# Performance work log

Measured on AMD Instinct MI355X. Metric: run time of the kernel, lower is better.

The kernel has to match this reference:

```python
import jax, jax.numpy as jnp
import numpy as np

D_MODEL = 1024
NUM_HEADS = 16
HEAD_DIM = D_MODEL // NUM_HEADS
FF_DIM = 4096
MAX_SEQ_LEN = 5000
EPS = 1e-5


def setup_inputs() -> dict:
    key = jax.random.key(0)
    ks = jax.random.split(key, 16)
    B, S = 2, 2048
    s = 0.02
    inp = {
        'x': jax.random.normal(ks[0], (B, S, D_MODEL), dtype=jnp.float32),
        'mask': jnp.ones((B, 1, S, S), dtype=jnp.int32),
        # attention projections (stored as (in, out); y = x @ W + b)
        'wq': jax.random.normal(ks[1], (D_MODEL, D_MODEL), jnp.float32) * s,
        'bq': jnp.zeros((D_MODEL,), jnp.float32),
        'wk': jax.random.normal(ks[2], (D_MODEL, D_MODEL), jnp.float32) * s,
        'bk': jnp.zeros((D_MODEL,), jnp.float32),
        'wv': jax.random.normal(ks[3], (D_MODEL, D_MODEL), jnp.float32) * s,
        'bv': jnp.zeros((D_MODEL,), jnp.float32),
        'wo': jax.random.normal(ks[4], (D_MODEL, D_MODEL), jnp.float32) * s,
        'bo': jnp.zeros((D_MODEL,), jnp.float32),
        # FFN
        'w1': jax.random.normal(ks[5], (D_MODEL, FF_DIM), jnp.float32) * s,
        'b1': jnp.zeros((FF_DIM,), jnp.float32),
        'w2': jax.random.normal(ks[6], (FF_DIM, D_MODEL), jnp.float32) * s,
        'b2': jnp.zeros((D_MODEL,), jnp.float32),
        # layer norms
        'g1': jnp.ones((D_MODEL,), jnp.float32),
        'be1': jnp.zeros((D_MODEL,), jnp.float32),
        'g2': jnp.ones((D_MODEL,), jnp.float32),
        'be2': jnp.zeros((D_MODEL,), jnp.float32),
        # relative position bias table: (2*max_seq_len-1, num_heads)
        'bias_table': jax.random.normal(ks[7], (2 * MAX_SEQ_LEN - 1, NUM_HEADS), jnp.float32) * s,
    }
    return inp


def _layer_norm(x, g, b):
    mu = jnp.mean(x, axis=-1, keepdims=True)
    var = jnp.mean(jnp.square(x - mu), axis=-1, keepdims=True)
    return (x - mu) / jnp.sqrt(var + EPS) * g + b


def reference(x, mask, wq, bq, wk, bk, wv, bv, wo, bo,
              w1, b1, w2, b2, g1, be1, g2, be2, bias_table):
    B, S, _ = x.shape
    # --- pre-norm attention block ---
    residual = x
    xn = _layer_norm(x, g1, be1)

    # relative position bias, computed on-the-fly: (S, S, H)
    coords = jnp.arange(S)
    rel = coords[:, None] - coords[None, :] + (MAX_SEQ_LEN - 1)
    rel = jnp.clip(rel, 0, 2 * MAX_SEQ_LEN - 2)
    rel_bias = bias_table[rel]  # (S, S, H)

    q = (xn @ wq + bq).reshape(B, S, NUM_HEADS, HEAD_DIM)
    k = (xn @ wk + bk).reshape(B, S, NUM_HEADS, HEAD_DIM)
    v = (xn @ wv + bv).reshape(B, S, NUM_HEADS, HEAD_DIM)

    scores = jnp.einsum('bqhd,bkhd->bhqk', q, k) / jnp.sqrt(jnp.float32(HEAD_DIM))
    # torch: scores + bias.unsqueeze(0).transpose(1,3) -> adds bias[k, q, h]
    scores = scores + jnp.transpose(rel_bias, (2, 1, 0))[None]
    scores = jnp.where(mask == 0, jnp.float32(-1e9), scores)
    attn = jax.nn.softmax(scores, axis=-1)
    ctx = jnp.einsum('bhqk,bkhd->bqhd', attn, v).reshape(B, S, D_MODEL)
    attn_out = ctx @ wo + bo
    x = residual + attn_out

    # --- pre-norm FFN block ---
    residual = x
    xn = _layer_norm(x, g2, be2)
    h = jax.nn.gelu(xn @ w1 + b1, approximate=False)
    x = residual + (h @ w2 + b2)
    return x
```

## Files before the change

kernel.cpp:

```cpp
#include <hip/hip_runtime.h>
#include <hip/hip_bf16.h>
#include <math.h>

#define S_LEN 2048
#define DM 1024
#define NH 16
#define HD 64
#define FF 4096
#define MAXSEQ 5000
#define QS 3072

typedef __attribute__((ext_vector_type(8))) short bf16x8;
typedef __attribute__((ext_vector_type(4))) float f32x4;

__device__ __forceinline__ void async_copy16(const void* g, void* l) {
    __builtin_amdgcn_global_load_lds(
        (const __attribute__((address_space(1))) void*)g,
        (__attribute__((address_space(3))) void*)l, 16, 0, 0);
}

__device__ __forceinline__ short f2bf_s(float v) {
    __hip_bfloat16 h = __float2bfloat16(v);
    return *reinterpret_cast<short*>(&h);
}

__device__ __forceinline__ float gelu_fast(float v) {
    float u = 0.7978845608f * (v + 0.044715f * v * v * v);
    float e = __expf(2.0f * u);
    float th = 1.0f - 2.0f / (e + 1.0f);
    return 0.5f * v * (1.0f + th);
}

__global__ __launch_bounds__(256) void ln_bf16_kernel(
    const float* __restrict__ x, const float* __restrict__ g,
    const float* __restrict__ be, __hip_bfloat16* __restrict__ out)
{
    int row = blockIdx.x;
    int t = threadIdx.x;
    const float* xr = x + (size_t)row * DM;
    float v[4];
    float s = 0.f, sq = 0.f;
#pragma unroll
    for (int i = 0; i < 4; i++) {
        v[i] = xr[t + 256 * i];
        s += v[i];
        sq += v[i] * v[i];
    }
    __shared__ float rs[256], rs2[256];
    rs[t] = s; rs2[t] = sq;
    __syncthreads();
    for (int off = 128; off > 0; off >>= 1) {
        if (t < off) { rs[t] += rs[t + off]; rs2[t] += rs2[t + off]; }
        __syncthreads();
    }
    float mu = rs[0] * (1.0f / DM);
    float var = rs2[0] * (1.0f / DM) - mu * mu;
    float rstd = rsqrtf(var + 1e-5f);
    __hip_bfloat16* orow = out + (size_t)row * DM;
#pragma unroll
    for (int i = 0; i < 4; i++) {
        int c = t + 256 * i;
        orow[c] = __float2bfloat16((v[i] - mu) * rstd * g[c] + be[c]);
    }
}

__global__ __launch_bounds__(256) void reduce_ln_kernel(
    const float* __restrict__ P0, const float* __restrict__ P1,
    const float* __restrict__ bo, const float* __restrict__ x,
    const float* __restrict__ g, const float* __restrict__ be,
    float* __restrict__ out, __hip_bfloat16* __restrict__ xn)
{
    int row = blockIdx.x;
    int t = threadIdx.x;
    size_t base = (size_t)row * DM;
    float v[4];
    float s = 0.f, sq = 0.f;
#pragma unroll
    for (int i = 0; i < 4; i++) {
        int c = t + 256 * i;
        float val = P0[base + c] + P1[base + c] + bo[c] + x[base + c];
        out[base + c] = val;
        v[i] = val;
        s += val;
        sq += val * val;
    }
    __shared__ float rs[256], rs2[256];
    rs[t] = s; rs2[t] = sq;
    __syncthreads();
    for (int off = 128; off > 0; off >>= 1) {
        if (t < off) { rs[t] += rs[t + off]; rs2[t] += rs2[t + off]; }
        __syncthreads();
    }
    float mu = rs[0] * (1.0f / DM);
    float var = rs2[0] * (1.0f / DM) - mu * mu;
    float rstd = rsqrtf(var + 1e-5f);
#pragma unroll
    for (int i = 0; i < 4; i++) {
        int c = t + 256 * i;
        xn[base + c] = __float2bfloat16((v[i] - mu) * rstd * g[c] + be[c]);
    }
}

__global__ __launch_bounds__(256) void reduce2_kernel(
    const float4* __restrict__ P0, const float4* __restrict__ P1,
    const float* __restrict__ b2, float* __restrict__ out)
{
    int f = blockIdx.x * 256 + threadIdx.x;
    float4 a = P0[f], b = P1[f];
    float4 r = ((const float4*)out)[f];
    float4 bb = ((const float4*)b2)[f & 255];
    float4 o;
    o.x = r.x + a.x + b.x + bb.x;
    o.y = r.y + a.y + b.y + bb.y;
    o.z = r.z + a.z + b.z + bb.z;
    o.w = r.w + a.w + b.w + bb.w;
    ((float4*)out)[f] = o;
}

__global__ __launch_bounds__(256) void prep_kernel(
    const float* __restrict__ wq, const float* __restrict__ wk,
    const float* __restrict__ wv, const float* __restrict__ wo,
    const float* __restrict__ w1, const float* __restrict__ w2,
    const float* __restrict__ bq, const float* __restrict__ bk,
    const float* __restrict__ bv,
    __hip_bfloat16* __restrict__ WqkvT, __hip_bfloat16* __restrict__ WoT,
    __hip_bfloat16* __restrict__ W1T, __hip_bfloat16* __restrict__ W2T,
    float* __restrict__ bqkv)
{
    int blk = blockIdx.x;
    if (blk >= 12288) {
        int i = (blk - 12288) * 256 + threadIdx.x;
        float v = (i < 1024) ? bq[i] : (i < 2048 ? bk[i - 1024] : bv[i - 2048]);
        bqkv[i] = v;
        return;
    }
    const float* W; __hip_bfloat16* Wt; int K, N, tbase;
    if (blk < 1024)      { W = wq; Wt = WqkvT;                      K = 1024; N = 1024; tbase = 0; }
    else if (blk < 2048) { W = wk; Wt = WqkvT + (size_t)1024 * DM;  K = 1024; N = 1024; tbase = 1024; }
    else if (blk < 3072) { W = wv; Wt = WqkvT + (size_t)2048 * DM;  K = 1024; N = 1024; tbase = 2048; }
    else if (blk < 4096) { W = wo; Wt = WoT;                        K = 1024; N = 1024; tbase = 3072; }
    else if (blk < 8192) { W = w1; Wt = W1T;                        K = 1024; N = 4096; tbase = 4096; }
    else                 { W = w2; Wt = W2T;                        K = 4096; N = 1024; tbase = 8192; }

    int tau = blk - tbase;
    int nt = tau % (N / 32), kt = tau / (N / 32);
    int n0 = nt * 32, k0 = kt * 32;

    __shared__ float tile[32][33];
    int c = threadIdx.x & 31, r = threadIdx.x >> 5;
#pragma unroll
    for (int i = 0; i < 32; i += 8)
        tile[r + i][c] = W[(size_t)(k0 + r + i) * N + n0 + c];
    __syncthreads();
#pragma unroll
    for (int i = 0; i < 32; i += 8)
        Wt[(size_t)(n0 + r + i) * K + k0 + c] = __float2bfloat16(tile[c][r + i]);
}

#define BM 128
#define BN 128
#define BK 64

__global__ __launch_bounds__(256) void gemm_bf16_kernel(
    const short* __restrict__ A, const short* __restrict__ Bt,
    const float* __restrict__ bias, const float* __restrict__ res,
    float* __restrict__ Cf, __hip_bfloat16* __restrict__ Cb,
    __hip_bfloat16* __restrict__ Qb, __hip_bfloat16* __restrict__ Kb,
    __hip_bfloat16* __restrict__ Vt,
    int M, int N, int K, int Klen, int mode, int gelu)
{
    __shared__ __align__(16) short As[BM * BK];
    __shared__ __align__(16) short Bs[BN * BK];

    int t = threadIdx.x;
    int l = t & 63;
    int m0 = blockIdx.y * BM, n0 = blockIdx.x * BN;
    int w = t >> 6;
    int wm = (w >> 1) * 64, wn = (w & 1) * 64;
    int kbase = blockIdx.z * Klen;
    float* Cfo = Cf + (size_t)blockIdx.z * M * N;

    f32x4 acc[4][4] = {};

    const int ktiles = Klen / BK;
    for (int kt = 0; kt < ktiles; kt++) {
        int k0 = kbase + kt * BK;
        __syncthreads();
#pragma unroll
        for (int i = 0; i < 4; i++) {
            int c = t + 256 * i;
            int crow = c >> 3;
            int ccol = ((c & 7) ^ (crow & 7)) * 8;
            int ldsoff = (c & ~63) * 8;
            async_copy16(A + (size_t)(m0 + crow) * K + k0 + ccol, As + ldsoff);
            async_copy16(Bt + (size_t)(n0 + crow) * K + k0 + ccol, Bs + ldsoff);
        }
        __syncthreads();

#pragma unroll
        for (int kb = 0; kb < 2; kb++) {
            bf16x8 af[4], bfr[4];
#pragma unroll
            for (int mt = 0; mt < 4; mt++) {
                int row = wm + mt * 16 + (l & 15);
                int j = (kb * 4 + (l >> 4)) ^ (row & 7);
                af[mt] = *(const bf16x8*)(As + row * BK + j * 8);
            }
#pragma unroll
            for (int nt = 0; nt < 4; nt++) {
                int row = wn + nt * 16 + (l & 15);
                int j = (kb * 4 + (l >> 4)) ^ (row & 7);
                bfr[nt] = *(const bf16x8*)(Bs + row * BK + j * 8);
            }
#pragma unroll
            for (int mt = 0; mt < 4; mt++)
#pragma unroll
                for (int nt = 0; nt < 4; nt++)
                    acc[mt][nt] = __builtin_amdgcn_mfma_f32_16x16x32_bf16(
                        af[mt], bfr[nt], acc[mt][nt], 0, 0, 0);
        }
    }

    int lc = l & 15, lr4 = (l >> 4) * 4;
    if (mode == 2) {
#pragma unroll
        for (int mt = 0; mt < 4; mt++) {
#pragma unroll
            for (int nt = 0; nt < 4; nt++) {
                int cg = n0 + wn + nt * 16 + lc;
                int mbase = m0 + wm + mt * 16 + lr4;
                int bb = mbase >> 11, seq0 = mbase & 2047;
                int sec = cg >> 10, d = cg & 63, hh = (cg >> 6) & 15;
                float bv = bias[cg];
                float vals[4];
#pragma unroll
                for (int r = 0; r < 4; r++) vals[r] = acc[mt][nt][r] + bv;
                if (sec == 0) {
                    __hip_bfloat16* p = Qb + ((size_t)(bb * NH + hh) * S_LEN + seq0) * HD + d;
#pragma unroll
                    for (int r = 0; r < 4; r++) p[r * HD] = __float2bfloat16(vals[r] * 0.125f);
                } else if (sec == 1) {
                    __hip_bfloat16* p = Kb + ((size_t)(bb * NH + hh) * S_LEN + seq0) * HD + d;
#pragma unroll
                    for (int r = 0; r < 4; r++) p[r * HD] = __float2bfloat16(vals[r]);
                } else {
                    ushort4 u;
                    u.x = (unsigned short)f2bf_s(vals[0]);
                    u.y = (unsigned short)f2bf_s(vals[1]);
                    u.z = (unsigned short)f2bf_s(vals[2]);
                    u.w = (unsigned short)f2bf_s(vals[3]);
                    *(ushort4*)(Vt + ((size_t)(bb * NH + hh) * HD + d) * S_LEN + seq0) = u;
                }
            }
        }
        return;
    }

#pragma unroll
    for (int mt = 0; mt < 4; mt++) {
#pragma unroll
        for (int nt = 0; nt < 4; nt++) {
            int col = n0 + wn + nt * 16 + lc;
            float bv = bias ? bias[col] : 0.f;
#pragma unroll
            for (int r = 0; r < 4; r++) {
                int row = m0 + wm + mt * 16 + lr4 + r;
                float v = acc[mt][nt][r] + bv;
                if (res) v += res[(size_t)row * N + col];
                if (gelu) v = gelu_fast(v);
                if (mode == 0) Cfo[(size_t)row * N + col] = v;
                else Cb[(size_t)row * N + col] = __float2bfloat16(v);
            }
        }
    }
}

__global__ __launch_bounds__(256) void attn_mfma_kernel(
    const __hip_bfloat16* __restrict__ Qb, const __hip_bfloat16* __restrict__ Kb,
    const __hip_bfloat16* __restrict__ Vt, const float* __restrict__ bias_table,
    __hip_bfloat16* __restrict__ ctx)
{
    int q0 = blockIdx.x * 64;
    int h = blockIdx.y, b = blockIdx.z;
    int t = threadIdx.x, l = t & 63, w = t >> 6;
    int lc = l & 15, lq = l >> 4;

    __shared__ __align__(16) short Ks[64 * 64];
    __shared__ __align__(16) short Vts[64 * 64];
    __shared__ __align__(16) short Ps[4][16 * 64];
    __shared__ float bias_s[128];

    const size_t bh = (size_t)b * NH + h;
    const short* Qh = (const short*)Qb + bh * (size_t)(S_LEN * HD);
    const short* Kh = (const short*)Kb + bh * (size_t)(S_LEN * HD);
    const short* Vh = (const short*)Vt + bh * (size_t)(S_LEN * HD);

    bf16x8 qf[2];
    {
        size_t qrow = (size_t)(q0 + w * 16 + lc) * HD;
        qf[0] = *(const bf16x8*)(Qh + qrow + lq * 8);
        qf[1] = *(const bf16x8*)(Qh + qrow + 32 + lq * 8);
    }

    float rsum[4] = {0.f, 0.f, 0.f, 0.f};
    f32x4 oacc[4] = {};

    for (int k0s = 0; k0s < S_LEN; k0s += 64) {
        __syncthreads();
#pragma unroll
        for (int i = 0; i < 2; i++) {
            int c = t + 256 * i;
            int row = c >> 3;
            int col = ((c & 7) ^ (row & 7)) * 8;
            int ldsoff = (c & ~63) * 8;
            async_copy16(Kh + (size_t)(k0s + row) * HD + col, Ks + ldsoff);
            async_copy16(Vh + (size_t)row * S_LEN + k0s + col, Vts + ldsoff);
        }
        if (t < 127)
            bias_s[t] = bias_table[(size_t)(k0s - q0 + (MAXSEQ - 1) + t - 63) * NH + h];
        __syncthreads();

        f32x4 sacc[4];
        int dbase = lc - (w * 16 + lq * 4) + 63;
#pragma unroll
        for (int ct = 0; ct < 4; ct++) {
            int di = dbase + ct * 16;
            f32x4 ci;
            ci[0] = bias_s[di];
            ci[1] = bias_s[di - 1];
            ci[2] = bias_s[di - 2];
            ci[3] = bias_s[di - 3];
            sacc[ct] = ci;
        }
#pragma unroll
        for (int ct = 0; ct < 4; ct++) {
            int row = ct * 16 + lc;
            bf16x8 b0 = *(const bf16x8*)(Ks + row * 64 + ((lq) ^ (row & 7)) * 8);
            bf16x8 b1 = *(const bf16x8*)(Ks + row * 64 + ((4 + lq) ^ (row & 7)) * 8);
            sacc[ct] = __builtin_amdgcn_mfma_f32_16x16x32_bf16(qf[0], b0, sacc[ct], 0, 0, 0);
            sacc[ct] = __builtin_amdgcn_mfma_f32_16x16x32_bf16(qf[1], b1, sacc[ct], 0, 0, 0);
        }

#pragma unroll
        for (int r = 0; r < 4; r++) {
            int rloc = lq * 4 + r;
#pragma unroll
            for (int ct = 0; ct < 4; ct++) {
                float p = __expf(sacc[ct][r]);
                rsum[r] += p;
                Ps[w][rloc * 64 + (((ct * 2 + (lc >> 3)) ^ (rloc & 7)) * 8) + (l & 7)] = f2bf_s(p);
            }
        }

        bf16x8 pf[2];
        pf[0] = *(const bf16x8*)(&Ps[w][lc * 64 + ((lq) ^ (lc & 7)) * 8]);
        pf[1] = *(const bf16x8*)(&Ps[w][lc * 64 + ((4 + lq) ^ (lc & 7)) * 8]);
#pragma unroll
        for (int dt = 0; dt < 4; dt++) {
            int row = dt * 16 + lc;
            bf16x8 v0 = *(const bf16x8*)(Vts + row * 64 + ((lq) ^ (row & 7)) * 8);
            bf16x8 v1 = *(const bf16x8*)(Vts + row * 64 + ((4 + lq) ^ (row & 7)) * 8);
            oacc[dt] = __builtin_amdgcn_mfma_f32_16x16x32_bf16(pf[0], v0, oacc[dt], 0, 0, 0);
            oacc[dt] = __builtin_amdgcn_mfma_f32_16x16x32_bf16(pf[1], v1, oacc[dt], 0, 0, 0);
        }
    }

#pragma unroll
    for (int r = 0; r < 4; r++) {
        float s = rsum[r];
        s += __shfl_xor(s, 1);
        s += __shfl_xor(s, 2);
        s += __shfl_xor(s, 4);
        s += __shfl_xor(s, 8);
        rsum[r] = 1.0f / s;
    }

#pragma unroll
    for (int r = 0; r < 4; r++) {
        size_t token = (size_t)b * S_LEN + q0 + w * 16 + lq * 4 + r;
#pragma unroll
        for (int dt = 0; dt < 4; dt++) {
            ctx[token * DM + h * HD + dt * 16 + lc] = __float2bfloat16(oacc[dt][r] * rsum[r]);
        }
    }
}

extern "C" void kernel_launch(void* const* d_in, const int* in_sizes, int n_in,
                              void* d_out, int out_size, void* d_ws, size_t ws_size,
                              hipStream_t stream)
{
    (void)in_sizes; (void)n_in; (void)out_size; (void)ws_size;

    const float* x  = (const float*)d_in[0];
    const float* wq = (const float*)d_in[2];
    const float* bq = (const float*)d_in[3];
    const float* wk = (const float*)d_in[4];
    const float* bk = (const float*)d_in[5];
    const float* wv = (const float*)d_in[6];
    const float* bv = (const float*)d_in[7];
    const float* wo = (const float*)d_in[8];
    const float* bo = (const float*)d_in[9];
    const float* w1 = (const float*)d_in[10];
    const float* b1 = (const float*)d_in[11];
    const float* w2 = (const float*)d_in[12];
    const float* b2 = (const float*)d_in[13];
    const float* g1 = (const float*)d_in[14];
    const float* be1 = (const float*)d_in[15];
    const float* g2 = (const float*)d_in[16];
    const float* be2 = (const float*)d_in[17];
    const float* bias_table = (const float*)d_in[18];

    float* out = (float*)d_out;
    const int BS = 2 * S_LEN;

    char* wsb = (char*)d_ws;
    const size_t MB = 1024 * 1024;
    __hip_bfloat16* Qb  = (__hip_bfloat16*)(wsb + 0 * MB);
    __hip_bfloat16* Kb  = (__hip_bfloat16*)(wsb + 8 * MB);
    __hip_bfloat16* Vt  = (__hip_bfloat16*)(wsb + 16 * MB);
    __hip_bfloat16* ctx = (__hip_bfloat16*)(wsb + 24 * MB);
    __hip_bfloat16* hbuf = (__hip_bfloat16*)(wsb + 0 * MB);
    __hip_bfloat16* xn1 = (__hip_bfloat16*)(wsb + 32 * MB);
    __hip_bfloat16* xn2 = xn1;
    __hip_bfloat16* WqkvT = (__hip_bfloat16*)(wsb + 40 * MB);
    __hip_bfloat16* WoT   = (__hip_bfloat16*)(wsb + 46 * MB);
    __hip_bfloat16* W1T   = (__hip_bfloat16*)(wsb + 48 * MB);
    __hip_bfloat16* W2T   = (__hip_bfloat16*)(wsb + 56 * MB);
    float* P0 = (float*)(wsb + 64 * MB);
    float* P1 = (float*)(wsb + 80 * MB);
    float* bqkv = (float*)(wsb + 64 * MB);

    dim3 blk(256);

    prep_kernel<<<dim3(12300), blk, 0, stream>>>(
        wq, wk, wv, wo, w1, w2, bq, bk, bv, WqkvT, WoT, W1T, W2T, bqkv);

    ln_bf16_kernel<<<dim3(BS), blk, 0, stream>>>(x, g1, be1, xn1);

    gemm_bf16_kernel<<<dim3(QS / BN, BS / BM), blk, 0, stream>>>(
        (const short*)xn1, (const short*)WqkvT, bqkv, nullptr, nullptr, nullptr,
        Qb, Kb, Vt, BS, QS, DM, DM, 2, 0);

    attn_mfma_kernel<<<dim3(S_LEN / 64, NH, 2), blk, 0, stream>>>(
        Qb, Kb, Vt, bias_table, ctx);

    gemm_bf16_kernel<<<dim3(DM / BN, BS / BM, 2), blk, 0, stream>>>(
        (const short*)ctx, (const short*)WoT, nullptr, nullptr, P0, nullptr,
        nullptr, nullptr, nullptr, BS, DM, DM, DM / 2, 0, 0);

    reduce_ln_kernel<<<dim3(BS), blk, 0, stream>>>(
        P0, P1, bo, x, g2, be2, out, xn2);

    gemm_bf16_kernel<<<dim3(FF / BN, BS / BM), blk, 0, stream>>>(
        (const short*)xn2, (const short*)W1T, b1, nullptr, nullptr, hbuf,
        nullptr, nullptr, nullptr, BS, FF, DM, DM, 1, 1);

    gemm_bf16_kernel<<<dim3(DM / BN, BS / BM, 2), blk, 0, stream>>>(
        (const short*)hbuf, (const short*)W2T, nullptr, nullptr, P0, nullptr,
        nullptr, nullptr, nullptr, BS, DM, FF, FF / 2, 0, 0);

    reduce2_kernel<<<dim3(4096), blk, 0, stream>>>(
        (const float4*)P0, (const float4*)P1, b2, out);
}
```

Baseline: 423.7 us.

## Double-buffer attention K/V tiles and keep P in registers via transposed MFMA

The attention kernel now double-buffers the K and V tiles with async global-to-LDS copies and waits on vmcnt, so the next tile loads while the current one is computed. It also swaps the MFMA operand order so the score accumulator layout feeds the P·V MFMA straight from registers, which removes the LDS round-trip for P. Scores are moved to base 2: Q is prescaled by log2(e)/8 and the bias is scaled by log2(e), so raw v_exp_f32 can be used. The whole relative-bias window is preloaded once into LDS as bf16, and output stores are vectorised. Risks include reduced bias precision from bf16 and no max-subtraction in the softmax (as before).

```diff
diff --git a/kernel.cpp b/kernel.cpp
--- a/kernel.cpp
+++ b/kernel.cpp
@@ -238,7 +238,7 @@
                 if (sec == 0) {
                     __hip_bfloat16* p = Qb + ((size_t)(bb * NH + hh) * S_LEN + seq0) * HD + d;
 #pragma unroll
-                    for (int r = 0; r < 4; r++) p[r * HD] = __float2bfloat16(vals[r] * 0.125f);
+                    for (int r = 0; r < 4; r++) p[r * HD] = __float2bfloat16(vals[r] * 0.1803368801f);
                 } else if (sec == 1) {
                     __hip_bfloat16* p = Kb + ((size_t)(bb * NH + hh) * S_LEN + seq0) * HD + d;
 #pragma unroll
@@ -275,7 +275,7 @@
     }
 }
 
-__global__ __launch_bounds__(256) void attn_mfma_kernel(
+__global__ __launch_bounds__(256, 4) void attn_mfma_kernel(
     const __hip_bfloat16* __restrict__ Qb, const __hip_bfloat16* __restrict__ Kb,
     const __hip_bfloat16* __restrict__ Vt, const float* __restrict__ bias_table,
     __hip_bfloat16* __restrict__ ctx)
@@ -285,15 +285,19 @@
     int t = threadIdx.x, l = t & 63, w = t >> 6;
     int lc = l & 15, lq = l >> 4;
 
-    __shared__ __align__(16) short Ks[64 * 64];
-    __shared__ __align__(16) short Vts[64 * 64];
-    __shared__ __align__(16) short Ps[4][16 * 64];
-    __shared__ float bias_s[128];
+    __shared__ __align__(16) short Ks[2][64 * 64];
+    __shared__ __align__(16) short Vts[2][64 * 64];
+    __shared__ unsigned short bias_u[2112];
 
     const size_t bh = (size_t)b * NH + h;
     const short* Qh = (const short*)Qb + bh * (size_t)(S_LEN * HD);
     const short* Kh = (const short*)Kb + bh * (size_t)(S_LEN * HD);
     const short* Vh = (const short*)Vt + bh * (size_t)(S_LEN * HD);
+
+    for (int i = t; i < 2111; i += 256) {
+        float v = bias_table[(size_t)(i - 63 - q0 + (MAXSEQ - 1)) * NH + h] * 1.44269504f;
+        bias_u[i] = (unsigned short)f2bf_s(v);
+    }
 
     bf16x8 qf[2];
     {
@@ -301,87 +305,103 @@
         qf[0] = *(const bf16x8*)(Qh + qrow + lq * 8);
         qf[1] = *(const bf16x8*)(Qh + qrow + 32 + lq * 8);
     }
-
-    float rsum[4] = {0.f, 0.f, 0.f, 0.f};
+    asm volatile("" : "+v"(qf[0]), "+v"(qf[1]));
+    asm volatile("s_waitcnt lgkmcnt(0)" ::: "memory");
+
+    float rsum = 0.f;
     f32x4 oacc[4] = {};
 
-    for (int k0s = 0; k0s < S_LEN; k0s += 64) {
-        __syncthreads();
+    auto stage = [&](int k0s, int bufi) {
 #pragma unroll
         for (int i = 0; i < 2; i++) {
             int c = t + 256 * i;
             int row = c >> 3;
-            int col = ((c & 7) ^ (row & 7)) * 8;
+            int fk = (row ^ (row >> 1)) & 7;
             int ldsoff = (c & ~63) * 8;
-            async_copy16(Kh + (size_t)(k0s + row) * HD + col, Ks + ldsoff);
-            async_copy16(Vh + (size_t)row * S_LEN + k0s + col, Vts + ldsoff);
-        }
-        if (t < 127)
-            bias_s[t] = bias_table[(size_t)(k0s - q0 + (MAXSEQ - 1) + t - 63) * NH + h];
-        __syncthreads();
-
+            async_copy16(Kh + (size_t)(k0s + row) * HD + ((c & 7) ^ fk) * 8,
+                         &Ks[bufi][ldsoff]);
+            async_copy16(Vh + (size_t)row * S_LEN + k0s + ((c & 7) ^ (row & 7)) * 8,
+                         &Vts[bufi][ldsoff]);
+        }
+    };
+
+    stage(0, 0);
+
+    for (int kt = 0; kt < S_LEN / 64; kt++) {
+        int cur = kt & 1;
+        int k0s = kt * 64;
+        if (kt < S_LEN / 64 - 1) {
+            stage(k0s + 64, cur ^ 1);
+            asm volatile("s_waitcnt vmcnt(4)" ::: "memory");
+        } else {
+            asm volatile("s_waitcnt vmcnt(0)" ::: "memory");
+        }
+        __builtin_amdgcn_s_barrier();
+
+        int jb = k0s + lq * 8 - (w * 16 + lc) + 63;
         f32x4 sacc[4];
-        int dbase = lc - (w * 16 + lq * 4) + 63;
+        __builtin_amdgcn_s_setprio(1);
 #pragma unroll
         for (int ct = 0; ct < 4; ct++) {
-            int di = dbase + ct * 16;
+            int kr = (ct >> 1) * 32 + (lc >> 2) * 8 + (ct & 1) * 4 + (lc & 3);
+            int fk = (kr ^ (kr >> 1)) & 7;
+            const short* kb = &Ks[cur][kr * 64];
+            bf16x8 k0 = *(const bf16x8*)(kb + ((lq ^ fk) * 8));
+            bf16x8 k1 = *(const bf16x8*)(kb + (((4 + lq) ^ fk) * 8));
+            int jj = jb + (ct >> 1) * 32 + (ct & 1) * 4;
             f32x4 ci;
-            ci[0] = bias_s[di];
-            ci[1] = bias_s[di - 1];
-            ci[2] = bias_s[di - 2];
-            ci[3] = bias_s[di - 3];
-            sacc[ct] = ci;
-        }
+#pragma unroll
+            for (int r = 0; r < 4; r++)
+                ci[r] = __uint_as_float((unsigned)bias_u[jj + r] << 16);
+            ci = __builtin_amdgcn_mfma_f32_16x16x32_bf16(k0, qf[0], ci, 0, 0, 0);
+            sacc[ct] = __builtin_amdgcn_mfma_f32_16x16x32_bf16(k1, qf[1], ci, 0, 0, 0);
+        }
+        __builtin_amdgcn_s_setprio(0);
+
+        int pks[8];
 #pragma unroll
         for (int ct = 0; ct < 4; ct++) {
-            int row = ct * 16 + lc;
-            bf16x8 b0 = *(const bf16x8*)(Ks + row * 64 + ((lq) ^ (row & 7)) * 8);
-            bf16x8 b1 = *(const bf16x8*)(Ks + row * 64 + ((4 + lq) ^ (row & 7)) * 8);
-            sacc[ct] = __builtin_amdgcn_mfma_f32_16x16x32_bf16(qf[0], b0, sacc[ct], 0, 0, 0);
-            sacc[ct] = __builtin_amdgcn_mfma_f32_16x16x32_bf16(qf[1], b1, sacc[ct], 0, 0, 0);
-        }
-
-#pragma unroll
-        for (int r = 0; r < 4; r++) {
-            int rloc = lq * 4 + r;
-#pragma unroll
-            for (int ct = 0; ct < 4; ct++) {
-                float p = __expf(sacc[ct][r]);
-                rsum[r] += p;
-                Ps[w][rloc * 64 + (((ct * 2 + (lc >> 3)) ^ (rloc & 7)) * 8) + (l & 7)] = f2bf_s(p);
-            }
-        }
-
-        bf16x8 pf[2];
-        pf[0] = *(const bf16x8*)(&Ps[w][lc * 64 + ((lq) ^ (lc & 7)) * 8]);
-        pf[1] = *(const bf16x8*)(&Ps[w][lc * 64 + ((4 + lq) ^ (lc & 7)) * 8]);
+            float p0, p1, p2, p3;
+            asm("v_exp_f32 %0, %1" : "=v"(p0) : "v"(sacc[ct][0]));
+            asm("v_exp_f32 %0, %1" : "=v"(p1) : "v"(sacc[ct][1]));
+            asm("v_exp_f32 %0, %1" : "=v"(p2) : "v"(sacc[ct][2]));
+            asm("v_exp_f32 %0, %1" : "=v"(p3) : "v"(sacc[ct][3]));
+            rsum += (p0 + p1) + (p2 + p3);
+            asm("v_cvt_pk_bf16_f32 %0, %1, %2" : "=v"(pks[ct * 2])     : "v"(p0), "v"(p1));
+            asm("v_cvt_pk_bf16_f32 %0, %1, %2" : "=v"(pks[ct * 2 + 1]) : "v"(p2), "v"(p3));
+        }
+        union { int i[4]; bf16x8 v; } pf0, pf1;
+#pragma unroll
+        for (int j = 0; j < 4; j++) { pf0.i[j] = pks[j]; pf1.i[j] = pks[4 + j]; }
+
+        __builtin_amdgcn_s_setprio(1);
 #pragma unroll
         for (int dt = 0; dt < 4; dt++) {
-            int row = dt * 16 + lc;
-            bf16x8 v0 = *(const bf16x8*)(Vts + row * 64 + ((lq) ^ (row & 7)) * 8);
-            bf16x8 v1 = *(const bf16x8*)(Vts + row * 64 + ((4 + lq) ^ (row & 7)) * 8);
-            oacc[dt] = __builtin_amdgcn_mfma_f32_16x16x32_bf16(pf[0], v0, oacc[dt], 0, 0, 0);
-            oacc[dt] = __builtin_amdgcn_mfma_f32_16x16x32_bf16(pf[1], v1, oacc[dt], 0, 0, 0);
-        }
-    }
-
-#pragma unroll
-    for (int r = 0; r < 4; r++) {
-        float s = rsum[r];
-        s += __shfl_xor(s, 1);
-        s += __shfl_xor(s, 2);
-        s += __shfl_xor(s, 4);
-        s += __shfl_xor(s, 8);
-        rsum[r] = 1.0f / s;
-    }
-
-#pragma unroll
-    for (int r = 0; r < 4; r++) {
-        size_t token = (size_t)b * S_LEN + q0 + w * 16 + lq * 4 + r;
-#pragma unroll
-        for (int dt = 0; dt < 4; dt++) {
-            ctx[token * DM + h * HD + dt * 16 + lc] = __float2bfloat16(oacc[dt][r] * rsum[r]);
-        }
+            int vr = dt * 16 + lc;
+            const short* vb = &Vts[cur][vr * 64];
+            bf16x8 v0 = *(const bf16x8*)(vb + ((lq ^ (vr & 7)) * 8));
+            bf16x8 v1 = *(const bf16x8*)(vb + (((4 + lq) ^ (vr & 7)) * 8));
+            oacc[dt] = __builtin_amdgcn_mfma_f32_16x16x32_bf16(v0, pf0.v, oacc[dt], 0, 0, 0);
+            oacc[dt] = __builtin_amdgcn_mfma_f32_16x16x32_bf16(v1, pf1.v, oacc[dt], 0, 0, 0);
+        }
+        __builtin_amdgcn_s_setprio(0);
+        __builtin_amdgcn_s_barrier();
+    }
+
+    rsum += __shfl_xor(rsum, 16);
+    rsum += __shfl_xor(rsum, 32);
+    float inv = 1.0f / rsum;
+
+    size_t tok = (size_t)b * S_LEN + q0 + w * 16 + lc;
+    __hip_bfloat16* cp = ctx + tok * DM + h * HD + lq * 4;
+#pragma unroll
+    for (int dt = 0; dt < 4; dt++) {
+        ushort4 u;
+        u.x = (unsigned short)f2bf_s(oacc[dt][0] * inv);
+        u.y = (unsigned short)f2bf_s(oacc[dt][1] * inv);
+        u.z = (unsigned short)f2bf_s(oacc[dt][2] * inv);
+        u.w = (unsigned short)f2bf_s(oacc[dt][3] * inv);
+        *(ushort4*)(cp + dt * 16) = u;
     }
 }
 
```

Result: no change. 419.7 us (-0.9%).
